# Kernel tuning notes

Hardware: AMD Instinct MI355X
Metric: run time of the kernel (lower is better)

Reference implementation:

```python
import jax, jax.numpy as jnp
import numpy as np

TAU = 2.0          # LIF membrane time constant (spikingjelly default)
VTH = 1.0          # spike threshold
LN_EPS = 1e-5
SEG_EPS = 1e-8


def layer_norm(x, g, b):
    m = jnp.mean(x, axis=-1, keepdims=True)
    v = jnp.var(x, axis=-1, keepdims=True)
    return (x - m) / jnp.sqrt(v + LN_EPS) * g + b


def setup_inputs() -> dict:
    key = jax.random.key(0)
    ks = jax.random.split(key, 12)
    B, T = 16, 2048
    V, D, DP, H, O = 256, 128, 768, 1024, 768
    s = 0.02
    inp = {
        'inputs': jax.random.randint(ks[0], (B, T), 0, V),
        'emb_table': jax.random.normal(ks[1], (V, D), jnp.float32) * s,
        'ctx_W': jax.random.normal(ks[2], (D, D), jnp.float32) * s,
        'ctx_b': jnp.zeros((D,), jnp.float32),
        'ctx_ln_g': jnp.ones((D,), jnp.float32),
        'ctx_ln_b': jnp.zeros((D,), jnp.float32),
        'bnd_W': jax.random.normal(ks[3], (D, 1), jnp.float32) * s,
        'bnd_b': jnp.zeros((1,), jnp.float32),
        'rst_W': jax.random.normal(ks[4], (D, 1), jnp.float32) * s,
        'rst_b': jnp.zeros((1,), jnp.float32),
        'proj_ln1_g': jnp.ones((D,), jnp.float32),
        'proj_ln1_b': jnp.zeros((D,), jnp.float32),
        'proj_W1': jax.random.normal(ks[5], (D, H), jnp.float32) * s,
        'proj_b1': jnp.zeros((H,), jnp.float32),
        'proj_W2': jax.random.normal(ks[6], (H, O), jnp.float32) * s,
        'proj_b2': jnp.zeros((O,), jnp.float32),
        'proj_ln2_g': jnp.ones((O,), jnp.float32),
        'proj_ln2_b': jnp.zeros((O,), jnp.float32),
    }
    return inp


def _forward(inputs, emb_table, ctx_W, ctx_b, ctx_ln_g, ctx_ln_b,
             bnd_W, bnd_b, rst_W, rst_b,
             proj_ln1_g, proj_ln1_b, proj_W1, proj_b1,
             proj_W2, proj_b2, proj_ln2_g, proj_ln2_b):
    # padding_idx=0: embedding row 0 is frozen zeros
    emb = emb_table.at[0].set(0.0)
    char_embs = emb[inputs]                                  # (B, T, D)
    h = jax.nn.gelu(layer_norm(char_embs @ ctx_W + ctx_b, ctx_ln_g, ctx_ln_b),
                    approximate=False)                       # (B, T, D)
    boundary_logits = jnp.tanh((h @ bnd_W + bnd_b)[..., 0])  # (B, T)
    reset_logits = (h @ rst_W + rst_b)[..., 0]               # (B, T)

    # Conditional LIF scan over time (multi-step mode): charge, record v,
    # spike, then hard-reset only where (spike & reset_mask).
    x_seq = boundary_logits.T                                # (T, B)
    reset_mask = (jax.nn.sigmoid(reset_logits) > 0.5).T      # (T, B) bool

    def step(v, xr):
        x, r = xr
        v = v + (x - v) / TAU                                # charge (decay_input, v_reset=0)
        s = v >= VTH
        v_next = jnp.where(s & r, 0.0, v)                    # conditional hard reset
        return v_next, (s.astype(v.dtype), v)                # record v pre-reset

    v0 = jnp.zeros_like(x_seq[0])
    _, (spikes, past_v) = jax.lax.scan(step, v0, (x_seq, reset_mask))
    soft_boundaries = past_v.T                               # (B, T) membrane potentials
    hard_boundaries = spikes.T                               # (B, T) 0/1 spikes

    # ---- segment pooling (torch builds dense BxTxK one-hot + einsum; here
    # we do the equivalent segment-sum directly) ----
    B, T, D = h.shape
    K = T  # static upper bound; torch's clamp(ids,0,K-1) is then a no-op
    ids = jnp.cumsum(hard_boundaries.astype(jnp.int32), axis=1)
    ids = jnp.roll(ids, 1, axis=1).at[:, 0].set(0)
    ids = jnp.clip(ids, 0, K - 1)                            # token_ids (B, T)

    w = jax.nn.relu(soft_boundaries)                         # (B, T)
    flat_ids = (ids + jnp.arange(B, dtype=ids.dtype)[:, None] * K).reshape(-1)
    num = jax.ops.segment_sum((w[..., None] * h).reshape(B * T, D),
                              flat_ids, num_segments=B * K).reshape(B, K, D)
    den = jax.ops.segment_sum(w.reshape(-1), flat_ids,
                              num_segments=B * K).reshape(B, K, 1)
    token_embs = num / (den + SEG_EPS)                       # (B, K, D)

    # projection MLP
    z = layer_norm(token_embs, proj_ln1_g, proj_ln1_b)
    z = jax.nn.gelu(z @ proj_W1 + proj_b1, approximate=False)
    z = z @ proj_W2 + proj_b2
    out = layer_norm(z, proj_ln2_g, proj_ln2_b)              # (B, K, 768)
    return out


def reference(inputs, emb_table, ctx_W, ctx_b, ctx_ln_g, ctx_ln_b,
              bnd_W, bnd_b, rst_W, rst_b,
              proj_ln1_g, proj_ln1_b, proj_W1, proj_b1,
              proj_W2, proj_b2, proj_ln2_g, proj_ln2_b):
    return _forward(inputs, emb_table, ctx_W, ctx_b, ctx_ln_g, ctx_ln_b,
                    bnd_W, bnd_b, rst_W, rst_b,
                    proj_ln1_g, proj_ln1_b, proj_W1, proj_b1,
                    proj_W2, proj_b2, proj_ln2_g, proj_ln2_b)
```

## Files before the change

kernel.cpp:

```cpp
#include <hip/hip_runtime.h>
#include <hip/hip_bf16.h>
#include <math.h>

#define NB 16
#define NT 2048
#define NR (NB*NT)
#define ND 128
#define NH 1024
#define NO 768
#define NK NT
#define K1_ROWS 32
#define NCH 32
#define TCH (NT/NCH)
#define SC_THREADS 256
#define SC_PER (NT/SC_THREADS)
#define R_FILL 32
#define RKR 16
#define RM1PB 16
#define RMAX1 (NB*RM1PB)
#define KCH 16

__device__ __forceinline__ float gelu_f(float x){
    return 0.5f * x * (1.0f + erff(x * 0.70710678118654752440f));
}
__device__ __forceinline__ void fma4(float4& a, float s, float4 w){
    a.x = fmaf(s, w.x, a.x);
    a.y = fmaf(s, w.y, a.y);
    a.z = fmaf(s, w.z, a.z);
    a.w = fmaf(s, w.w, a.w);
}

__global__ __launch_bounds__(256) void k_embed_ctx(
    const int* __restrict__ inp, const float* __restrict__ emb,
    const float* __restrict__ Wc, const float* __restrict__ bc,
    const float* __restrict__ lng, const float* __restrict__ lnb,
    const float* __restrict__ bndW, const float* __restrict__ bndB,
    const float* __restrict__ rstW, const float* __restrict__ rstB,
    float* __restrict__ hout, float* __restrict__ xseq, int* __restrict__ rmask)
{
    __shared__ float sE[K1_ROWS][ND];
    const int tid = threadIdx.x;
    const int r0 = blockIdx.x * K1_ROWS;

    #pragma unroll
    for (int q = 0; q < 4; q++){
        int fidx = tid + 256*q;
        int row  = fidx >> 5;
        int c4   = fidx & 31;
        int tokv = inp[r0 + row];
        float4 ev = make_float4(0.f, 0.f, 0.f, 0.f);
        if (tokv != 0) ev = ((const float4*)emb)[tokv*(ND/4) + c4];
        ((float4*)(&sE[row][0]))[c4] = ev;
    }
    __syncthreads();

    const int bun  = tid >> 5;
    const int lane = tid & 31;
    const int jo   = lane * 4;
    const int rbse = bun * 4;

    float4 acc0 = make_float4(0,0,0,0);
    float4 acc1 = acc0, acc2 = acc0, acc3 = acc0;

    for (int k0 = 0; k0 < ND; k0 += 4){
        float4 e0 = *(const float4*)&sE[rbse+0][k0];
        float4 e1 = *(const float4*)&sE[rbse+1][k0];
        float4 e2 = *(const float4*)&sE[rbse+2][k0];
        float4 e3 = *(const float4*)&sE[rbse+3][k0];
        float4 w0 = *(const float4*)&Wc[(k0+0)*ND + jo];
        float4 w1 = *(const float4*)&Wc[(k0+1)*ND + jo];
        float4 w2 = *(const float4*)&Wc[(k0+2)*ND + jo];
        float4 w3 = *(const float4*)&Wc[(k0+3)*ND + jo];
        fma4(acc0, e0.x, w0); fma4(acc0, e0.y, w1); fma4(acc0, e0.z, w2); fma4(acc0, e0.w, w3);
        fma4(acc1, e1.x, w0); fma4(acc1, e1.y, w1); fma4(acc1, e1.z, w2); fma4(acc1, e1.w, w3);
        fma4(acc2, e2.x, w0); fma4(acc2, e2.y, w1); fma4(acc2, e2.z, w2); fma4(acc2, e2.w, w3);
        fma4(acc3, e3.x, w0); fma4(acc3, e3.y, w1); fma4(acc3, e3.z, w2); fma4(acc3, e3.w, w3);
    }

    const float4 cb  = ((const float4*)bc)[lane];
    const float4 gv  = ((const float4*)lng)[lane];
    const float4 bv  = ((const float4*)lnb)[lane];
    const float4 bwv = ((const float4*)bndW)[lane];
    const float4 rwv = ((const float4*)rstW)[lane];
    const float bb0 = bndB[0], rr0 = rstB[0];

    #define K1_EPI(ACC, RR) do { \
        float4 a = ACC; \
        a.x += cb.x; a.y += cb.y; a.z += cb.z; a.w += cb.w; \
        float s_ = a.x + a.y + a.z + a.w; \
        float q_ = a.x*a.x + a.y*a.y + a.z*a.z + a.w*a.w; \
        for (int off = 16; off > 0; off >>= 1){ s_ += __shfl_xor(s_, off, 32); q_ += __shfl_xor(q_, off, 32); } \
        float m_ = s_ * (1.0f/ND); \
        float rstd_ = rsqrtf(q_ * (1.0f/ND) - m_*m_ + 1e-5f); \
        float4 hh; \
        hh.x = gelu_f((a.x - m_)*rstd_*gv.x + bv.x); \
        hh.y = gelu_f((a.y - m_)*rstd_*gv.y + bv.y); \
        hh.z = gelu_f((a.z - m_)*rstd_*gv.z + bv.z); \
        hh.w = gelu_f((a.w - m_)*rstd_*gv.w + bv.w); \
        *(float4*)&hout[(size_t)(r0 + rbse + RR)*ND + jo] = hh; \
        float pb = hh.x*bwv.x + hh.y*bwv.y + hh.z*bwv.z + hh.w*bwv.w; \
        float pr = hh.x*rwv.x + hh.y*rwv.y + hh.z*rwv.z + hh.w*rwv.w; \
        for (int off = 16; off > 0; off >>= 1){ pb += __shfl_xor(pb, off, 32); pr += __shfl_xor(pr, off, 32); } \
        if (lane == 0){ \
            int rg = r0 + rbse + RR; \
            xseq[rg]  = tanhf(pb + bb0); \
            rmask[rg] = (pr + rr0) > 0.f ? 1 : 0; \
        } \
    } while(0)

    K1_EPI(acc0, 0); K1_EPI(acc1, 1); K1_EPI(acc2, 2); K1_EPI(acc3, 3);
    #undef K1_EPI
}

__global__ __launch_bounds__(SC_THREADS) void k_scan(
    const float* __restrict__ x, const int* __restrict__ rm,
    float* __restrict__ wout, int* __restrict__ ids, int* __restrict__ used)
{
    const int b   = blockIdx.x;
    const int tid = threadIdx.x;
    const int t0  = tid * SC_PER;

    float xv[SC_PER];
    int   rv[SC_PER];
    {
        const float4* xb4 = (const float4*)(x + b*NT + t0);
        float4 xa = xb4[0], xb = xb4[1];
        xv[0]=xa.x; xv[1]=xa.y; xv[2]=xa.z; xv[3]=xa.w;
        xv[4]=xb.x; xv[5]=xb.y; xv[6]=xb.z; xv[7]=xb.w;
        const int4* rb4 = (const int4*)(rm + b*NT + t0);
        int4 r0_ = rb4[0], r1_ = rb4[1];
        rv[0]=r0_.x; rv[1]=r0_.y; rv[2]=r0_.z; rv[3]=r0_.w;
        rv[4]=r1_.x; rv[5]=r1_.y; rv[6]=r1_.z; rv[7]=r1_.w;
    }

    __shared__ float sA[SC_THREADS], sB[SC_THREADS];
    __shared__ float sA2[SC_THREADS], sB2[SC_THREADS];
    __shared__ int   smin;

    float vkeep[SC_PER];
    #pragma unroll
    for (int i = 0; i < SC_PER; i++) vkeep[i] = 0.f;

    int s = 0;
    while (true){
        float aL = 1.f, bL = 0.f;
        #pragma unroll
        for (int i = 0; i < SC_PER; i++){
            if (t0 + i >= s){
                aL *= 0.5f;
                bL = 0.5f*(bL + xv[i]);
            }
        }
        sA[tid] = aL; sB[tid] = bL;
        __syncthreads();
        float *Ain = sA, *Bin = sB, *Aout = sA2, *Bout = sB2;
        for (int off = 1; off < SC_THREADS; off <<= 1){
            float a_cur = Ain[tid], b_cur = Bin[tid];
            float a_pre = 1.f, b_pre = 0.f;
            if (tid >= off){ a_pre = Ain[tid-off]; b_pre = Bin[tid-off]; }
            Aout[tid] = a_pre * a_cur;
            Bout[tid] = fmaf(a_cur, b_pre, b_cur);
            __syncthreads();
            float* t1 = Ain; Ain = Aout; Aout = t1;
            float* t2 = Bin; Bin = Bout; Bout = t2;
        }
        float v = (tid == 0) ? 0.f : Bin[tid-1];
        int cand = NT;
        #pragma unroll
        for (int i = 0; i < SC_PER; i++){
            if (t0 + i >= s){
                v = 0.5f*(v + xv[i]);
                vkeep[i] = v;
                if (v >= 1.0f && rv[i] && cand == NT) cand = t0 + i;
            }
        }
        if (tid == 0) smin = NT;
        __syncthreads();
        if (cand < NT) atomicMin(&smin, cand);
        __syncthreads();
        int tmin = smin;
        __syncthreads();
        if (tmin >= NT) break;
        s = tmin + 1;
    }

    int sp[SC_PER]; int cnt_loc = 0;
    #pragma unroll
    for (int i = 0; i < SC_PER; i++){ sp[i] = (vkeep[i] >= 1.0f) ? 1 : 0; cnt_loc += sp[i]; }

    __shared__ int sI[SC_THREADS], sI2[SC_THREADS];
    sI[tid] = cnt_loc;
    __syncthreads();
    int *Iin = sI, *Iout = sI2;
    for (int off = 1; off < SC_THREADS; off <<= 1){
        int vcur = Iin[tid];
        int vpre = (tid >= off) ? Iin[tid-off] : 0;
        Iout[tid] = vcur + vpre;
        __syncthreads();
        int* tt = Iin; Iin = Iout; Iout = tt;
    }
    int c = (tid == 0) ? 0 : Iin[tid-1];

    float wv_[SC_PER]; int id_[SC_PER];
    #pragma unroll
    for (int i = 0; i < SC_PER; i++){
        id_[i] = (c < NK-1) ? c : (NK-1);
        wv_[i] = fmaxf(vkeep[i], 0.f);
        c += sp[i];
    }
    float4* w4 = (float4*)(wout + b*NT + t0);
    w4[0] = make_float4(wv_[0], wv_[1], wv_[2], wv_[3]);
    w4[1] = make_float4(wv_[4], wv_[5], wv_[6], wv_[7]);
    int4* i4 = (int4*)(ids + b*NT + t0);
    i4[0] = make_int4(id_[0], id_[1], id_[2], id_[3]);
    i4[1] = make_int4(id_[4], id_[5], id_[6], id_[7]);
    if (tid == SC_THREADS-1) used[b] = id_[SC_PER-1] + 1;
}

__global__ __launch_bounds__(128) void k_pool_part(
    const float* __restrict__ h, const float* __restrict__ w,
    const int* __restrict__ ids, float* __restrict__ tok,
    float* __restrict__ pnum, float* __restrict__ pden, int* __restrict__ pid)
{
    const int c   = blockIdx.x;
    const int b   = blockIdx.y;
    const int tid = threadIdx.x;
    const int t0  = c * TCH;

    __shared__ int   sid[TCH];
    __shared__ float swt[TCH];
    if (tid < TCH){
        sid[tid] = ids[b*NT + t0 + tid];
        swt[tid] = w  [b*NT + t0 + tid];
    }
    float hbuf[TCH];
    #pragma unroll
    for (int i = 0; i < TCH; i++)
        hbuf[i] = h[((size_t)(b*NT + t0 + i))*ND + tid];
    __syncthreads();

    const int ebase = (b*NCH + c)*2;
    float acc = 0.f, den = 0.f;
    int   cur = sid[0];
    bool  flushed = false;
    #pragma unroll
    for (int i = 0; i < TCH; i++){
        int id = sid[i];
        if (id != cur){
            if (!flushed){
                pnum[(size_t)ebase*ND + tid] = acc;
                if (tid == 0){ pden[ebase] = den; pid[ebase] = cur; }
                flushed = true;
            } else {
                tok[((size_t)(b*NK + cur))*ND + tid] = acc / (den + 1e-8f);
            }
            acc = 0.f; den = 0.f; cur = id;
        }
        acc = fmaf(swt[i], hbuf[i], acc);
        den += swt[i];
    }
    if (!flushed){
        pnum[(size_t)ebase*ND + tid] = acc;
        if (tid == 0){ pden[ebase] = den; pid[ebase] = cur; pid[ebase+1] = -1; }
    } else {
        pnum[((size_t)ebase+1)*ND + tid] = acc;
        if (tid == 0){ pden[ebase+1] = den; pid[ebase+1] = cur; }
    }
}

__global__ __launch_bounds__(128) void k_pool_combine(
    const float* __restrict__ pnum, const float* __restrict__ pden,
    const int* __restrict__ pid, float* __restrict__ tok)
{
    const int b   = blockIdx.x;
    const int tid = threadIdx.x;
    int cur = -1; float acc = 0.f, den = 0.f;
    for (int e = 0; e < NCH*2; e++){
        const int gi = b*NCH*2 + e;
        int id = pid[gi];
        if (id < 0) continue;
        float nv = pnum[(size_t)gi*ND + tid];
        float dv = pden[gi];
        if (id == cur){ acc += nv; den += dv; }
        else {
            if (cur >= 0) tok[((size_t)(b*NK + cur))*ND + tid] = acc / (den + 1e-8f);
            cur = id; acc = nv; den = dv;
        }
    }
    if (cur >= 0) tok[((size_t)(b*NK + cur))*ND + tid] = acc / (den + 1e-8f);
}

__global__ __launch_bounds__(256) void k_empty_u(
    const float* __restrict__ ln1b, const float* __restrict__ W1,
    const float* __restrict__ b1, float* __restrict__ uvec)
{
    __shared__ float z[ND];
    const int tid = threadIdx.x;
    const int j = blockIdx.x * 256 + tid;
    if (tid < ND) z[tid] = ln1b[tid];
    __syncthreads();
    float a = b1[j];
    #pragma unroll 16
    for (int k = 0; k < ND; k++)
        a = fmaf(z[k], W1[(size_t)k*NH + j], a);
    uvec[j] = gelu_f(a);
}

__global__ __launch_bounds__(256) void k_empty_mv(
    const float* __restrict__ uvec, const float* __restrict__ W2,
    float* __restrict__ pvec_part)
{
    __shared__ float su[256];
    __shared__ float part[4][64];
    const int tid = threadIdx.x;
    const int colbase = blockIdx.x * 64;
    const int kq = blockIdx.y;
    const int ksub = tid >> 6;
    const int col  = tid & 63;
    su[tid] = uvec[kq*256 + tid];
    __syncthreads();
    float p = 0.f;
    #pragma unroll 8
    for (int k = ksub*64; k < ksub*64 + 64; k++)
        p = fmaf(su[k], W2[(size_t)(kq*256 + k)*NO + colbase + col], p);
    part[ksub][col] = p;
    __syncthreads();
    if (tid < 64)
        pvec_part[kq*NO + colbase + tid] =
            part[0][tid] + part[1][tid] + part[2][tid] + part[3][tid];
}

__global__ __launch_bounds__(256) void k_empty_fin(
    const float* __restrict__ pvec_part, const float* __restrict__ b2,
    const float* __restrict__ g2, const float* __restrict__ lb2,
    float* __restrict__ cvec)
{
    __shared__ float red[8];
    const int tid = threadIdx.x;
    float p0 = b2[tid      ], p1 = b2[tid + 256], p2 = b2[tid + 512];
    #pragma unroll
    for (int q = 0; q < 4; q++){
        p0 += pvec_part[q*NO + tid      ];
        p1 += pvec_part[q*NO + tid + 256];
        p2 += pvec_part[q*NO + tid + 512];
    }
    float s = p0+p1+p2, qq = p0*p0 + p1*p1 + p2*p2;
    for (int off = 32; off > 0; off >>= 1){ s += __shfl_xor(s, off); qq += __shfl_xor(qq, off); }
    if ((tid & 63) == 0){ red[tid>>6] = s; red[4 + (tid>>6)] = qq; }
    __syncthreads();
    s  = red[0]+red[1]+red[2]+red[3];
    qq = red[4]+red[5]+red[6]+red[7];
    float m = s * (1.0f/NO);
    float rstd = rsqrtf(qq * (1.0f/NO) - m*m + 1e-5f);
    cvec[tid      ] = (p0 - m)*rstd*g2[tid      ] + lb2[tid      ];
    cvec[tid + 256] = (p1 - m)*rstd*g2[tid + 256] + lb2[tid + 256];
    cvec[tid + 512] = (p2 - m)*rstd*g2[tid + 512] + lb2[tid + 512];
}

__global__ void k_rows(const int* __restrict__ used, int* __restrict__ rmeta,
                       int* __restrict__ rlist)
{
    if (threadIdx.x == 0){
        int n = 0;
        for (int b = 0; b < NB; b++){
            int u = used[b]; int m = u < RM1PB ? u : RM1PB;
            for (int k = 0; k < m; k++) rlist[n++] = (b<<16) | k;
        }
        rmeta[0] = n;
    }
}

__global__ __launch_bounds__(256) void k_ureal(
    const int* __restrict__ rmeta, const int* __restrict__ rlist,
    const float* __restrict__ tok,
    const float* __restrict__ ln1g, const float* __restrict__ ln1b,
    const float* __restrict__ W1, const float* __restrict__ b1,
    float* __restrict__ ubuf)
{
    const int i = blockIdx.x;
    if (i >= rmeta[0]) return;
    const int q   = blockIdx.y;
    const int tid = threadIdx.x;
    const int bk  = rlist[i];
    const int b = bk >> 16, k = bk & 0xffff;

    __shared__ float zz[ND];
    __shared__ float red[8];
    float tv = 0.f, s = 0.f, qq = 0.f;
    if (tid < ND){
        tv = tok[((size_t)(b*NK + k))*ND + tid];
        s = tv; qq = tv*tv;
    }
    for (int off = 32; off > 0; off >>= 1){ s += __shfl_xor(s, off); qq += __shfl_xor(qq, off); }
    if ((tid & 63) == 0){ red[tid>>6] = s; red[4 + (tid>>6)] = qq; }
    __syncthreads();
    s  = red[0]+red[1]+red[2]+red[3];
    qq = red[4]+red[5]+red[6]+red[7];
    float m = s * (1.0f/ND);
    float rstd = rsqrtf(qq * (1.0f/ND) - m*m + 1e-5f);
    if (tid < ND) zz[tid] = (tv - m)*rstd*ln1g[tid] + ln1b[tid];
    __syncthreads();

    const int j = q*256 + tid;
    float a = b1[j];
    #pragma unroll 8
    for (int kk = 0; kk < ND; kk++)
        a = fmaf(zz[kk], W1[(size_t)kk*NH + j], a);
    ubuf[(size_t)i*NH + j] = gelu_f(a);
}

__global__ __launch_bounds__(256) void k_preal(
    const int* __restrict__ rmeta, const float* __restrict__ ubuf,
    const float* __restrict__ W2, float* __restrict__ pbuf)
{
    const int cb  = blockIdx.x;
    const int kc  = blockIdx.y;
    const int tid = threadIdx.x;
    const int ksub = tid >> 6;
    const int col  = tid & 63;
    const int R1 = rmeta[0];
    const int colg  = cb*64 + col;
    const int kbase = kc*64 + ksub*16;

    float w2v[16];
    #pragma unroll
    for (int t = 0; t < 16; t++)
        w2v[t] = W2[(size_t)(kbase + t)*NO + colg];

    __shared__ float part[4][64];
    for (int i = 0; i < R1; i++){
        const float* ui = ubuf + (size_t)i*NH + kbase;
        float p = 0.f;
        #pragma unroll
        for (int t = 0; t < 16; t++) p = fmaf(ui[t], w2v[t], p);
        part[ksub][col] = p;
        __syncthreads();
        if (ksub == 0)
            pbuf[((size_t)kc*RMAX1 + i)*NO + colg] =
                part[0][col] + part[1][col] + part[2][col] + part[3][col];
        __syncthreads();
    }
}

__global__ __launch_bounds__(256) void k_finreal(
    const int* __restrict__ rmeta, const int* __restrict__ rlist,
    const float* __restrict__ pbuf, const float* __restrict__ b2,
    const float* __restrict__ g2, const float* __restrict__ lb2,
    float* __restrict__ out)
{
    const int i = blockIdx.x;
    if (i >= rmeta[0]) return;
    const int tid = threadIdx.x;
    const int bk  = rlist[i];
    const int b = bk >> 16, k = bk & 0xffff;

    __shared__ float red[8];
    float p0 = b2[tid], p1 = b2[tid+256], p2 = b2[tid+512];
    #pragma unroll
    for (int kc = 0; kc < KCH; kc++){
        const float* pp = pbuf + ((size_t)kc*RMAX1 + i)*NO;
        p0 += pp[tid]; p1 += pp[tid+256]; p2 += pp[tid+512];
    }
    float s = p0+p1+p2, qq = p0*p0 + p1*p1 + p2*p2;
    for (int off = 32; off > 0; off >>= 1){ s += __shfl_xor(s, off); qq += __shfl_xor(qq, off); }
    if ((tid & 63) == 0){ red[tid>>6] = s; red[4 + (tid>>6)] = qq; }
    __syncthreads();
    s  = red[0]+red[1]+red[2]+red[3];
    qq = red[4]+red[5]+red[6]+red[7];
    float m = s * (1.0f/NO);
    float rstd = rsqrtf(qq * (1.0f/NO) - m*m + 1e-5f);
    float* orow = out + ((size_t)(b*NK + k))*NO;
    orow[tid      ] = (p0 - m)*rstd*g2[tid      ] + lb2[tid      ];
    orow[tid + 256] = (p1 - m)*rstd*g2[tid + 256] + lb2[tid + 256];
    orow[tid + 512] = (p2 - m)*rstd*g2[tid + 512] + lb2[tid + 512];
}

__global__ __launch_bounds__(192) void k_fill(
    const float* __restrict__ cvec, float* __restrict__ out)
{
    const int tid = threadIdx.x;
    const size_t r0 = (size_t)blockIdx.x * R_FILL;
    const float4 cv = ((const float4*)cvec)[tid];
    float4* o4 = (float4*)out + r0*(NO/4) + tid;
    #pragma unroll
    for (int r = 0; r < R_FILL; r++)
        o4[(size_t)r*(NO/4)] = cv;
}

__global__ __launch_bounds__(256) void k_mlp_tail(
    const float* __restrict__ tok, const int* __restrict__ used,
    const float* __restrict__ ln1g, const float* __restrict__ ln1b,
    const float* __restrict__ W1, const float* __restrict__ b1,
    const float* __restrict__ W2, const float* __restrict__ b2,
    const float* __restrict__ g2, const float* __restrict__ lb2,
    float* __restrict__ out)
{
    __shared__ float zz[ND];
    __shared__ float su[NH];
    __shared__ float red[8];
    const int tid = threadIdx.x;
    const int b   = blockIdx.y;
    const int k0  = RM1PB + blockIdx.x * RKR;
    const int u   = used[b];
    if (k0 >= u) return;

    for (int kr = 0; kr < RKR; kr++){
        const int k = k0 + kr;
        if (k >= u) break;
        float* orow = out + ((size_t)(b*NK + k)) * NO;

        float tv = 0.f, s = 0.f, qq = 0.f;
        if (tid < ND){
            tv = tok[((size_t)(b*NK + k))*ND + tid];
            s = tv; qq = tv*tv;
        }
        for (int off = 32; off > 0; off >>= 1){ s += __shfl_xor(s, off); qq += __shfl_xor(qq, off); }
        if ((tid & 63) == 0){ red[tid>>6] = s; red[4 + (tid>>6)] = qq; }
        __syncthreads();
        s  = red[0]+red[1]+red[2]+red[3];
        qq = red[4]+red[5]+red[6]+red[7];
        float m = s * (1.0f/ND);
        float rstd = rsqrtf(qq * (1.0f/ND) - m*m + 1e-5f);
        if (tid < ND) zz[tid] = (tv - m)*rstd*ln1g[tid] + ln1b[tid];
        __syncthreads();

        float4 a = ((const float4*)b1)[tid];
        for (int kk = 0; kk < ND; kk++)
            fma4(a, zz[kk], ((const float4*)W1)[kk*(NH/4) + tid]);
        float4 gg;
        gg.x = gelu_f(a.x); gg.y = gelu_f(a.y); gg.z = gelu_f(a.z); gg.w = gelu_f(a.w);
        ((float4*)su)[tid] = gg;
        __syncthreads();

        float p0 = b2[tid], p1 = b2[tid+256], p2 = b2[tid+512];
        for (int kk = 0; kk < NH; kk++){
            float uk = su[kk];
            p0 = fmaf(uk, W2[kk*NO + tid      ], p0);
            p1 = fmaf(uk, W2[kk*NO + tid + 256], p1);
            p2 = fmaf(uk, W2[kk*NO + tid + 512], p2);
        }
        s = p0+p1+p2; qq = p0*p0 + p1*p1 + p2*p2;
        for (int off = 32; off > 0; off >>= 1){ s += __shfl_xor(s, off); qq += __shfl_xor(qq, off); }
        if ((tid & 63) == 0){ red[tid>>6] = s; red[4 + (tid>>6)] = qq; }
        __syncthreads();
        s  = red[0]+red[1]+red[2]+red[3];
        qq = red[4]+red[5]+red[6]+red[7];
        m = s * (1.0f/NO);
        rstd = rsqrtf(qq * (1.0f/NO) - m*m + 1e-5f);
        orow[tid      ] = (p0 - m)*rstd*g2[tid      ] + lb2[tid      ];
        orow[tid + 256] = (p1 - m)*rstd*g2[tid + 256] + lb2[tid + 256];
        orow[tid + 512] = (p2 - m)*rstd*g2[tid + 512] + lb2[tid + 512];
        __syncthreads();
    }
}

extern "C" void kernel_launch(void* const* d_in, const int* in_sizes, int n_in,
                              void* d_out, int out_size, void* d_ws, size_t ws_size,
                              hipStream_t stream)
{
    const int*   inp  = (const int*)  d_in[0];
    const float* emb  = (const float*)d_in[1];
    const float* Wc   = (const float*)d_in[2];
    const float* bc   = (const float*)d_in[3];
    const float* lng  = (const float*)d_in[4];
    const float* lnb  = (const float*)d_in[5];
    const float* bndW = (const float*)d_in[6];
    const float* bndB = (const float*)d_in[7];
    const float* rstW = (const float*)d_in[8];
    const float* rstB = (const float*)d_in[9];
    const float* g1   = (const float*)d_in[10];
    const float* b1l  = (const float*)d_in[11];
    const float* W1   = (const float*)d_in[12];
    const float* b1   = (const float*)d_in[13];
    const float* W2   = (const float*)d_in[14];
    const float* b2   = (const float*)d_in[15];
    const float* g2   = (const float*)d_in[16];
    const float* lb2  = (const float*)d_in[17];

    char* ws = (char*)d_ws;
    float* h    = (float*)(ws + 0);
    float* xq   = (float*)(ws + 16777216);
    int*   rm   = (int*)  (ws + 16908288);
    float* wv   = (float*)(ws + 17039360);
    int*   ids  = (int*)  (ws + 17170432);
    int*   usd  = (int*)  (ws + 17301504);
    float* cvec = (float*)(ws + 17301760);
    float* tok  = (float*)(ws + 17304832);
    float* pnum = (float*)(ws + 34082048);
    float* pden = (float*)(ws + 34606336);
    int*   pid  = (int*)  (ws + 34610432);
    float* uvec  = (float*)(ws + 16777216);
    float* pvpt  = (float*)(ws + 16777216 + 4096);
    int*   rmeta = (int*)  (ws + 16777216 + 16384);
    int*   rlist = (int*)  (ws + 16777216 + 16640);
    float* ubuf = (float*)(ws + 0);
    float* pbuf = (float*)(ws + 1048576);

    float* out = (float*)d_out;

    k_embed_ctx<<<dim3(NR / K1_ROWS), dim3(256), 0, stream>>>(
        inp, emb, Wc, bc, lng, lnb, bndW, bndB, rstW, rstB, h, xq, rm);
    k_scan<<<dim3(NB), dim3(SC_THREADS), 0, stream>>>(xq, rm, wv, ids, usd);
    k_pool_part<<<dim3(NCH, NB), dim3(128), 0, stream>>>(
        h, wv, ids, tok, pnum, pden, pid);
    k_pool_combine<<<dim3(NB), dim3(128), 0, stream>>>(pnum, pden, pid, tok);
    k_rows<<<dim3(1), dim3(64), 0, stream>>>(usd, rmeta, rlist);
    k_empty_u<<<dim3(NH/256), dim3(256), 0, stream>>>(b1l, W1, b1, uvec);
    k_empty_mv<<<dim3(NO/64, 4), dim3(256), 0, stream>>>(uvec, W2, pvpt);
    k_empty_fin<<<dim3(1), dim3(256), 0, stream>>>(pvpt, b2, g2, lb2, cvec);
    k_ureal<<<dim3(RMAX1, 4), dim3(256), 0, stream>>>(
        rmeta, rlist, tok, g1, b1l, W1, b1, ubuf);
    k_preal<<<dim3(NO/64, KCH), dim3(256), 0, stream>>>(rmeta, ubuf, W2, pbuf);
    k_fill<<<dim3(NR / R_FILL), dim3(192), 0, stream>>>(cvec, out);
    k_finreal<<<dim3(RMAX1), dim3(256), 0, stream>>>(
        rmeta, rlist, pbuf, b2, g2, lb2, out);
    k_mlp_tail<<<dim3((NK - RM1PB) / RKR, NB), dim3(256), 0, stream>>>(
        tok, usd, g1, b1l, W1, b1, W2, b2, g2, lb2, out);
}
```

Before: 238.5 us.

## Merge empty-token MLP path into real-row kernels and enlarge embed tile

Folds the constant empty-segment MLP vector computation into the real-row kernels as an extra row index, removing k_rows, k_empty_u, k_empty_mv and k_empty_fin launches. Real-row outputs now go to a staging buffer and are scattered after the fill. The embed/context kernel processes 64 rows per block with 8 accumulators per thread to reuse weight loads more. The combine kernel stages ids and denominators in shared memory. This cuts launch count, but adds a scatter kernel and uses more registers in the embed kernel.

```diff
diff --git a/kernel.cpp b/kernel.cpp
--- a/kernel.cpp
+++ b/kernel.cpp
@@ -9,7 +9,7 @@
 #define NH 1024
 #define NO 768
 #define NK NT
-#define K1_ROWS 32
+#define K1_ROWS 64
 #define NCH 32
 #define TCH (NT/NCH)
 #define SC_THREADS 256
@@ -43,7 +43,7 @@
     const int r0 = blockIdx.x * K1_ROWS;
 
     #pragma unroll
-    for (int q = 0; q < 4; q++){
+    for (int q = 0; q < 8; q++){
         int fidx = tid + 256*q;
         int row  = fidx >> 5;
         int c4   = fidx & 31;
@@ -57,24 +57,23 @@
     const int bun  = tid >> 5;
     const int lane = tid & 31;
     const int jo   = lane * 4;
-    const int rbse = bun * 4;
-
-    float4 acc0 = make_float4(0,0,0,0);
-    float4 acc1 = acc0, acc2 = acc0, acc3 = acc0;
+    const int rbse = bun * 8;
+
+    float4 acc[8];
+    #pragma unroll
+    for (int r = 0; r < 8; r++) acc[r] = make_float4(0,0,0,0);
 
     for (int k0 = 0; k0 < ND; k0 += 4){
-        float4 e0 = *(const float4*)&sE[rbse+0][k0];
-        float4 e1 = *(const float4*)&sE[rbse+1][k0];
-        float4 e2 = *(const float4*)&sE[rbse+2][k0];
-        float4 e3 = *(const float4*)&sE[rbse+3][k0];
         float4 w0 = *(const float4*)&Wc[(k0+0)*ND + jo];
         float4 w1 = *(const float4*)&Wc[(k0+1)*ND + jo];
         float4 w2 = *(const float4*)&Wc[(k0+2)*ND + jo];
         float4 w3 = *(const float4*)&Wc[(k0+3)*ND + jo];
-        fma4(acc0, e0.x, w0); fma4(acc0, e0.y, w1); fma4(acc0, e0.z, w2); fma4(acc0, e0.w, w3);
-        fma4(acc1, e1.x, w0); fma4(acc1, e1.y, w1); fma4(acc1, e1.z, w2); fma4(acc1, e1.w, w3);
-        fma4(acc2, e2.x, w0); fma4(acc2, e2.y, w1); fma4(acc2, e2.z, w2); fma4(acc2, e2.w, w3);
-        fma4(acc3, e3.x, w0); fma4(acc3, e3.y, w1); fma4(acc3, e3.z, w2); fma4(acc3, e3.w, w3);
+        #pragma unroll
+        for (int r = 0; r < 8; r++){
+            float4 e = *(const float4*)&sE[rbse+r][k0];
+            fma4(acc[r], e.x, w0); fma4(acc[r], e.y, w1);
+            fma4(acc[r], e.z, w2); fma4(acc[r], e.w, w3);
+        }
     }
 
     const float4 cb  = ((const float4*)bc)[lane];
@@ -84,32 +83,34 @@
     const float4 rwv = ((const float4*)rstW)[lane];
     const float bb0 = bndB[0], rr0 = rstB[0];
 
-    #define K1_EPI(ACC, RR) do { \
-        float4 a = ACC; \
-        a.x += cb.x; a.y += cb.y; a.z += cb.z; a.w += cb.w; \
-        float s_ = a.x + a.y + a.z + a.w; \
-        float q_ = a.x*a.x + a.y*a.y + a.z*a.z + a.w*a.w; \
-        for (int off = 16; off > 0; off >>= 1){ s_ += __shfl_xor(s_, off, 32); q_ += __shfl_xor(q_, off, 32); } \
-        float m_ = s_ * (1.0f/ND); \
-        float rstd_ = rsqrtf(q_ * (1.0f/ND) - m_*m_ + 1e-5f); \
-        float4 hh; \
-        hh.x = gelu_f((a.x - m_)*rstd_*gv.x + bv.x); \
-        hh.y = gelu_f((a.y - m_)*rstd_*gv.y + bv.y); \
-        hh.z = gelu_f((a.z - m_)*rstd_*gv.z + bv.z); \
-        hh.w = gelu_f((a.w - m_)*rstd_*gv.w + bv.w); \
-        *(float4*)&hout[(size_t)(r0 + rbse + RR)*ND + jo] = hh; \
-        float pb = hh.x*bwv.x + hh.y*bwv.y + hh.z*bwv.z + hh.w*bwv.w; \
-        float pr = hh.x*rwv.x + hh.y*rwv.y + hh.z*rwv.z + hh.w*rwv.w; \
-        for (int off = 16; off > 0; off >>= 1){ pb += __shfl_xor(pb, off, 32); pr += __shfl_xor(pr, off, 32); } \
-        if (lane == 0){ \
-            int rg = r0 + rbse + RR; \
-            xseq[rg]  = tanhf(pb + bb0); \
-            rmask[rg] = (pr + rr0) > 0.f ? 1 : 0; \
-        } \
-    } while(0)
-
-    K1_EPI(acc0, 0); K1_EPI(acc1, 1); K1_EPI(acc2, 2); K1_EPI(acc3, 3);
-    #undef K1_EPI
+    #pragma unroll
+    for (int r = 0; r < 8; r++){
+        float4 a = acc[r];
+        a.x += cb.x; a.y += cb.y; a.z += cb.z; a.w += cb.w;
+        float s_ = a.x + a.y + a.z + a.w;
+        float q_ = a.x*a.x + a.y*a.y + a.z*a.z + a.w*a.w;
+        for (int off = 16; off > 0; off >>= 1){
+            s_ += __shfl_xor(s_, off, 32); q_ += __shfl_xor(q_, off, 32);
+        }
+        float m_ = s_ * (1.0f/ND);
+        float rstd_ = rsqrtf(q_ * (1.0f/ND) - m_*m_ + 1e-5f);
+        float4 hh;
+        hh.x = gelu_f((a.x - m_)*rstd_*gv.x + bv.x);
+        hh.y = gelu_f((a.y - m_)*rstd_*gv.y + bv.y);
+        hh.z = gelu_f((a.z - m_)*rstd_*gv.z + bv.z);
+        hh.w = gelu_f((a.w - m_)*rstd_*gv.w + bv.w);
+        *(float4*)&hout[(size_t)(r0 + rbse + r)*ND + jo] = hh;
+        float pb = hh.x*bwv.x + hh.y*bwv.y + hh.z*bwv.z + hh.w*bwv.w;
+        float pr = hh.x*rwv.x + hh.y*rwv.y + hh.z*rwv.z + hh.w*rwv.w;
+        for (int off = 16; off > 0; off >>= 1){
+            pb += __shfl_xor(pb, off, 32); pr += __shfl_xor(pr, off, 32);
+        }
+        if (lane == 0){
+            int rg = r0 + rbse + r;
+            xseq[rg]  = tanhf(pb + bb0);
+            rmask[rg] = (pr + rr0) > 0.f ? 1 : 0;
+        }
+    }
 }
 
 __global__ __launch_bounds__(SC_THREADS) void k_scan(
@@ -274,13 +275,19 @@
 {
     const int b   = blockIdx.x;
     const int tid = threadIdx.x;
+    __shared__ int   spid[NCH*2];
+    __shared__ float spden[NCH*2];
+    if (tid < NCH*2){
+        spid[tid]  = pid [b*NCH*2 + tid];
+        spden[tid] = pden[b*NCH*2 + tid];
+    }
+    __syncthreads();
     int cur = -1; float acc = 0.f, den = 0.f;
     for (int e = 0; e < NCH*2; e++){
-        const int gi = b*NCH*2 + e;
-        int id = pid[gi];
+        int id = spid[e];
         if (id < 0) continue;
-        float nv = pnum[(size_t)gi*ND + tid];
-        float dv = pden[gi];
+        float nv = pnum[(size_t)(b*NCH*2 + e)*ND + tid];
+        float dv = spden[e];
         if (id == cur){ acc += nv; den += dv; }
         else {
             if (cur >= 0) tok[((size_t)(b*NK + cur))*ND + tid] = acc / (den + 1e-8f);
@@ -290,59 +297,106 @@
     if (cur >= 0) tok[((size_t)(b*NK + cur))*ND + tid] = acc / (den + 1e-8f);
 }
 
-__global__ __launch_bounds__(256) void k_empty_u(
-    const float* __restrict__ ln1b, const float* __restrict__ W1,
-    const float* __restrict__ b1, float* __restrict__ uvec)
-{
-    __shared__ float z[ND];
-    const int tid = threadIdx.x;
-    const int j = blockIdx.x * 256 + tid;
-    if (tid < ND) z[tid] = ln1b[tid];
-    __syncthreads();
+__global__ __launch_bounds__(256) void k_ureal(
+    const int* __restrict__ used, const float* __restrict__ tok,
+    const float* __restrict__ ln1g, const float* __restrict__ ln1b,
+    const float* __restrict__ W1, const float* __restrict__ b1,
+    float* __restrict__ ubuf)
+{
+    const int i   = blockIdx.x;
+    const int q   = blockIdx.y;
+    const int tid = threadIdx.x;
+    __shared__ float zz[ND];
+    __shared__ float red[8];
+
+    if (i < RMAX1){
+        const int b = i >> 4, k = i & 15;
+        int u = used[b]; if (u > RM1PB) u = RM1PB;
+        if (k >= u) return;
+        float tv = 0.f, s = 0.f, qq = 0.f;
+        if (tid < ND){
+            tv = tok[((size_t)(b*NK + k))*ND + tid];
+            s = tv; qq = tv*tv;
+        }
+        for (int off = 32; off > 0; off >>= 1){ s += __shfl_xor(s, off); qq += __shfl_xor(qq, off); }
+        if ((tid & 63) == 0){ red[tid>>6] = s; red[4 + (tid>>6)] = qq; }
+        __syncthreads();
+        s  = red[0]+red[1]+red[2]+red[3];
+        qq = red[4]+red[5]+red[6]+red[7];
+        float m = s * (1.0f/ND);
+        float rstd = rsqrtf(qq * (1.0f/ND) - m*m + 1e-5f);
+        if (tid < ND) zz[tid] = (tv - m)*rstd*ln1g[tid] + ln1b[tid];
+        __syncthreads();
+    } else {
+        if (tid < ND) zz[tid] = ln1b[tid];
+        __syncthreads();
+    }
+
+    const int j = q*256 + tid;
     float a = b1[j];
-    #pragma unroll 16
-    for (int k = 0; k < ND; k++)
-        a = fmaf(z[k], W1[(size_t)k*NH + j], a);
-    uvec[j] = gelu_f(a);
-}
-
-__global__ __launch_bounds__(256) void k_empty_mv(
-    const float* __restrict__ uvec, const float* __restrict__ W2,
-    float* __restrict__ pvec_part)
-{
-    __shared__ float su[256];
-    __shared__ float part[4][64];
-    const int tid = threadIdx.x;
-    const int colbase = blockIdx.x * 64;
-    const int kq = blockIdx.y;
+    #pragma unroll 8
+    for (int kk = 0; kk < ND; kk++)
+        a = fmaf(zz[kk], W1[(size_t)kk*NH + j], a);
+    ubuf[(size_t)i*NH + j] = gelu_f(a);
+}
+
+__global__ __launch_bounds__(256) void k_preal(
+    const int* __restrict__ used, const float* __restrict__ ubuf,
+    const float* __restrict__ W2, float* __restrict__ pbuf)
+{
+    const int cb  = blockIdx.x;
+    const int kc  = blockIdx.y;
+    const int tid = threadIdx.x;
     const int ksub = tid >> 6;
     const int col  = tid & 63;
-    su[tid] = uvec[kq*256 + tid];
+    const int colg  = cb*64 + col;
+    const int kbase = kc*64 + ksub*16;
+
+    __shared__ int susd[NB];
+    if (tid < NB){ int u = used[tid]; susd[tid] = u > RM1PB ? RM1PB : u; }
+
+    float w2v[16];
+    #pragma unroll
+    for (int t = 0; t < 16; t++)
+        w2v[t] = W2[(size_t)(kbase + t)*NO + colg];
+
+    __shared__ float part[4][64];
     __syncthreads();
-    float p = 0.f;
-    #pragma unroll 8
-    for (int k = ksub*64; k < ksub*64 + 64; k++)
-        p = fmaf(su[k], W2[(size_t)(kq*256 + k)*NO + colbase + col], p);
-    part[ksub][col] = p;
-    __syncthreads();
-    if (tid < 64)
-        pvec_part[kq*NO + colbase + tid] =
-            part[0][tid] + part[1][tid] + part[2][tid] + part[3][tid];
-}
-
-__global__ __launch_bounds__(256) void k_empty_fin(
-    const float* __restrict__ pvec_part, const float* __restrict__ b2,
-    const float* __restrict__ g2, const float* __restrict__ lb2,
+
+    for (int i = 0; i <= RMAX1; i++){
+        if (i < RMAX1 && (i & 15) >= susd[i >> 4]) continue;
+        const float* ui = ubuf + (size_t)i*NH + kbase;
+        float p = 0.f;
+        #pragma unroll
+        for (int t = 0; t < 16; t++) p = fmaf(ui[t], w2v[t], p);
+        part[ksub][col] = p;
+        __syncthreads();
+        if (ksub == 0)
+            pbuf[((size_t)kc*(RMAX1+1) + i)*NO + colg] =
+                part[0][col] + part[1][col] + part[2][col] + part[3][col];
+        __syncthreads();
+    }
+}
+
+__global__ __launch_bounds__(256) void k_fin(
+    const int* __restrict__ used, const float* __restrict__ pbuf,
+    const float* __restrict__ b2, const float* __restrict__ g2,
+    const float* __restrict__ lb2, float* __restrict__ rowst,
     float* __restrict__ cvec)
 {
+    const int i = blockIdx.x;
+    const int tid = threadIdx.x;
+    if (i < RMAX1){
+        const int b = i >> 4, k = i & 15;
+        int u = used[b]; if (u > RM1PB) u = RM1PB;
+        if (k >= u) return;
+    }
     __shared__ float red[8];
-    const int tid = threadIdx.x;
-    float p0 = b2[tid      ], p1 = b2[tid + 256], p2 = b2[tid + 512];
-    #pragma unroll
-    for (int q = 0; q < 4; q++){
-        p0 += pvec_part[q*NO + tid      ];
-        p1 += pvec_part[q*NO + tid + 256];
-        p2 += pvec_part[q*NO + tid + 512];
+    float p0 = b2[tid], p1 = b2[tid+256], p2 = b2[tid+512];
+    #pragma unroll
+    for (int kc = 0; kc < KCH; kc++){
+        const float* pp = pbuf + ((size_t)kc*(RMAX1+1) + i)*NO;
+        p0 += pp[tid]; p1 += pp[tid+256]; p2 += pp[tid+512];
     }
     float s = p0+p1+p2, qq = p0*p0 + p1*p1 + p2*p2;
     for (int off = 32; off > 0; off >>= 1){ s += __shfl_xor(s, off); qq += __shfl_xor(qq, off); }
@@ -352,127 +406,10 @@
     qq = red[4]+red[5]+red[6]+red[7];
     float m = s * (1.0f/NO);
     float rstd = rsqrtf(qq * (1.0f/NO) - m*m + 1e-5f);
-    cvec[tid      ] = (p0 - m)*rstd*g2[tid      ] + lb2[tid      ];
-    cvec[tid + 256] = (p1 - m)*rstd*g2[tid + 256] + lb2[tid + 256];
-    cvec[tid + 512] = (p2 - m)*rstd*g2[tid + 512] + lb2[tid + 512];
-}
-
-__global__ void k_rows(const int* __restrict__ used, int* __restrict__ rmeta,
-                       int* __restrict__ rlist)
-{
-    if (threadIdx.x == 0){
-        int n = 0;
-        for (int b = 0; b < NB; b++){
-            int u = used[b]; int m = u < RM1PB ? u : RM1PB;
-            for (int k = 0; k < m; k++) rlist[n++] = (b<<16) | k;
-        }
-        rmeta[0] = n;
-    }
-}
-
-__global__ __launch_bounds__(256) void k_ureal(
-    const int* __restrict__ rmeta, const int* __restrict__ rlist,
-    const float* __restrict__ tok,
-    const float* __restrict__ ln1g, const float* __restrict__ ln1b,
-    const float* __restrict__ W1, const float* __restrict__ b1,
-    float* __restrict__ ubuf)
-{
-    const int i = blockIdx.x;
-    if (i >= rmeta[0]) return;
-    const int q   = blockIdx.y;
-    const int tid = threadIdx.x;
-    const int bk  = rlist[i];
-    const int b = bk >> 16, k = bk & 0xffff;
-
-    __shared__ float zz[ND];
-    __shared__ float red[8];
-    float tv = 0.f, s = 0.f, qq = 0.f;
-    if (tid < ND){
-        tv = tok[((size_t)(b*NK + k))*ND + tid];
-        s = tv; qq = tv*tv;
-    }
-    for (int off = 32; off > 0; off >>= 1){ s += __shfl_xor(s, off); qq += __shfl_xor(qq, off); }
-    if ((tid & 63) == 0){ red[tid>>6] = s; red[4 + (tid>>6)] = qq; }
-    __syncthreads();
-    s  = red[0]+red[1]+red[2]+red[3];
-    qq = red[4]+red[5]+red[6]+red[7];
-    float m = s * (1.0f/ND);
-    float rstd = rsqrtf(qq * (1.0f/ND) - m*m + 1e-5f);
-    if (tid < ND) zz[tid] = (tv - m)*rstd*ln1g[tid] + ln1b[tid];
-    __syncthreads();
-
-    const int j = q*256 + tid;
-    float a = b1[j];
-    #pragma unroll 8
-    for (int kk = 0; kk < ND; kk++)
-        a = fmaf(zz[kk], W1[(size_t)kk*NH + j], a);
-    ubuf[(size_t)i*NH + j] = gelu_f(a);
-}
-
-__global__ __launch_bounds__(256) void k_preal(
-    const int* __restrict__ rmeta, const float* __restrict__ ubuf,
-    const float* __restrict__ W2, float* __restrict__ pbuf)
-{
-    const int cb  = blockIdx.x;
-    const int kc  = blockIdx.y;
-    const int tid = threadIdx.x;
-    const int ksub = tid >> 6;
-    const int col  = tid & 63;
-    const int R1 = rmeta[0];
-    const int colg  = cb*64 + col;
-    const int kbase = kc*64 + ksub*16;
-
-    float w2v[16];
-    #pragma unroll
-    for (int t = 0; t < 16; t++)
-        w2v[t] = W2[(size_t)(kbase + t)*NO + colg];
-
-    __shared__ float part[4][64];
-    for (int i = 0; i < R1; i++){
-        const float* ui = ubuf + (size_t)i*NH + kbase;
-        float p = 0.f;
-        #pragma unroll
-        for (int t = 0; t < 16; t++) p = fmaf(ui[t], w2v[t], p);
-        part[ksub][col] = p;
-        __syncthreads();
-        if (ksub == 0)
-            pbuf[((size_t)kc*RMAX1 + i)*NO + colg] =
-                part[0][col] + part[1][col] + part[2][col] + part[3][col];
-        __syncthreads();
-    }
-}
-
-__global__ __launch_bounds__(256) void k_finreal(
-    const int* __restrict__ rmeta, const int* __restrict__ rlist,
-    const float* __restrict__ pbuf, const float* __restrict__ b2,
-    const float* __restrict__ g2, const float* __restrict__ lb2,
-    float* __restrict__ out)
-{
-    const int i = blockIdx.x;
-    if (i >= rmeta[0]) return;
-    const int tid = threadIdx.x;
-    const int bk  = rlist[i];
-    const int b = bk >> 16, k = bk & 0xffff;
-
-    __shared__ float red[8];
-    float p0 = b2[tid], p1 = b2[tid+256], p2 = b2[tid+512];
-    #pragma unroll
-    for (int kc = 0; kc < KCH; kc++){
-        const float* pp = pbuf + ((size_t)kc*RMAX1 + i)*NO;
-        p0 += pp[tid]; p1 += pp[tid+256]; p2 += pp[tid+512];
-    }
-    float s = p0+p1+p2, qq = p0*p0 + p1*p1 + p2*p2;
-    for (int off = 32; off > 0; off >>= 1){ s += __shfl_xor(s, off); qq += __shfl_xor(qq, off); }
-    if ((tid & 63) == 0){ red[tid>>6] = s; red[4 + (tid>>6)] = qq; }
-    __syncthreads();
-    s  = red[0]+red[1]+red[2]+red[3];
-    qq = red[4]+red[5]+red[6]+red[7];
-    float m = s * (1.0f/NO);
-    float rstd = rsqrtf(qq * (1.0f/NO) - m*m + 1e-5f);
-    float* orow = out + ((size_t)(b*NK + k))*NO;
-    orow[tid      ] = (p0 - m)*rstd*g2[tid      ] + lb2[tid      ];
-    orow[tid + 256] = (p1 - m)*rstd*g2[tid + 256] + lb2[tid + 256];
-    orow[tid + 512] = (p2 - m)*rstd*g2[tid + 512] + lb2[tid + 512];
+    float* dst = (i < RMAX1) ? (rowst + (size_t)i*NO) : cvec;
+    dst[tid      ] = (p0 - m)*rstd*g2[tid      ] + lb2[tid      ];
+    dst[tid + 256] = (p1 - m)*rstd*g2[tid + 256] + lb2[tid + 256];
+    dst[tid + 512] = (p2 - m)*rstd*g2[tid + 512] + lb2[tid + 512];
 }
 
 __global__ __launch_bounds__(192) void k_fill(
@@ -485,6 +422,19 @@
     #pragma unroll
     for (int r = 0; r < R_FILL; r++)
         o4[(size_t)r*(NO/4)] = cv;
+}
+
+__global__ __launch_bounds__(192) void k_scatter(
+    const int* __restrict__ used, const float* __restrict__ rowst,
+    float* __restrict__ out)
+{
+    const int i = blockIdx.x;
+    const int b = i >> 4, k = i & 15;
+    int u = used[b]; if (u > RM1PB) u = RM1PB;
+    if (k >= u) return;
+    const int tid = threadIdx.x;
+    ((float4*)(out + ((size_t)(b*NK + k))*NO))[tid] =
+        ((const float4*)(rowst + (size_t)i*NO))[tid];
 }
 
 __global__ __launch_bounds__(256) void k_mlp_tail(
@@ -589,12 +539,9 @@
     float* pnum = (float*)(ws + 34082048);
     float* pden = (float*)(ws + 34606336);
     int*   pid  = (int*)  (ws + 34610432);
-    float* uvec  = (float*)(ws + 16777216);
-    float* pvpt  = (float*)(ws + 16777216 + 4096);
-    int*   rmeta = (int*)  (ws + 16777216 + 16384);
-    int*   rlist = (int*)  (ws + 16777216 + 16640);
-    float* ubuf = (float*)(ws + 0);
-    float* pbuf = (float*)(ws + 1048576);
+    float* ubuf  = (float*)(ws + 0);
+    float* pbuf  = (float*)(ws + 1052672);
+    float* rowst = (float*)(ws + 13684736);
 
     float* out = (float*)d_out;
 
@@ -604,16 +551,13 @@
     k_pool_part<<<dim3(NCH, NB), dim3(128), 0, stream>>>(
         h, wv, ids, tok, pnum, pden, pid);
     k_pool_combine<<<dim3(NB), dim3(128), 0, stream>>>(pnum, pden, pid, tok);
-    k_rows<<<dim3(1), dim3(64), 0, stream>>>(usd, rmeta, rlist);
-    k_empty_u<<<dim3(NH/256), dim3(256), 0, stream>>>(b1l, W1, b1, uvec);
-    k_empty_mv<<<dim3(NO/64, 4), dim3(256), 0, stream>>>(uvec, W2, pvpt);
-    k_empty_fin<<<dim3(1), dim3(256), 0, stream>>>(pvpt, b2, g2, lb2, cvec);
-    k_ureal<<<dim3(RMAX1, 4), dim3(256), 0, stream>>>(
-        rmeta, rlist, tok, g1, b1l, W1, b1, ubuf);
-    k_preal<<<dim3(NO/64, KCH), dim3(256), 0, stream>>>(rmeta, ubuf, W2, pbuf);
+    k_ureal<<<dim3(RMAX1+1, 4), dim3(256), 0, stream>>>(
+        usd, tok, g1, b1l, W1, b1, ubuf);
+    k_preal<<<dim3(NO/64, KCH), dim3(256), 0, stream>>>(usd, ubuf, W2, pbuf);
+    k_fin<<<dim3(RMAX1+1), dim3(256), 0, stream>>>(
+        usd, pbuf, b2, g2, lb2, rowst, cvec);
     k_fill<<<dim3(NR / R_FILL), dim3(192), 0, stream>>>(cvec, out);
-    k_finreal<<<dim3(RMAX1), dim3(256), 0, stream>>>(
-        rmeta, rlist, pbuf, b2, g2, lb2, out);
+    k_scatter<<<dim3(RMAX1), dim3(192), 0, stream>>>(usd, rowst, out);
     k_mlp_tail<<<dim3((NK - RM1PB) / RKR, NB), dim3(256), 0, stream>>>(
         tok, usd, g1, b1l, W1, b1, W2, b2, g2, lb2, out);
 }
```

After: 240.1 us. No clear change (+0.7%).
